# Kernel optimization log

Measured on AMD Instinct MI355X. Metric: run time of the kernel, lower is better.

The kernel has to match this reference:

```python
import jax, jax.numpy as jnp
import numpy as np

B, D, E, H1, H2 = 64, 2048, 64, 512, 256
EPS = 1e-5


def setup_inputs() -> dict:
    key = jax.random.key(0)
    ks = jax.random.split(key, 8)
    s = lambda k, shape, scale: jax.random.normal(k, shape, dtype=jnp.float32) * scale
    return {
        "sparse_representation": s(ks[0], (B, D), 1.0),
        "emb": s(ks[1], (D, E), 1.0),
        "W1": s(ks[2], (D + E, H1), (D + E) ** -0.5),
        "b1": s(ks[3], (H1,), 0.02),
        "g1": jnp.ones((H1,), jnp.float32),
        "beta1": jnp.zeros((H1,), jnp.float32),
        "m1": jnp.zeros((H1,), jnp.float32),
        "v1": jnp.ones((H1,), jnp.float32),
        "W2": s(ks[4], (H1, H2), H1 ** -0.5),
        "b2": s(ks[5], (H2,), 0.02),
        "g2": jnp.ones((H2,), jnp.float32),
        "beta2": jnp.zeros((H2,), jnp.float32),
        "m2": jnp.zeros((H2,), jnp.float32),
        "v2": jnp.ones((H2,), jnp.float32),
        "W3": s(ks[6], (H2, 1), H2 ** -0.5),
        "b3": s(ks[7], (1,), 0.02),
    }


def _bn_relu(x, g, beta, m, v):
    # eval-mode BatchNorm1d followed by ReLU
    return jax.nn.relu((x - m) * jax.lax.rsqrt(v + EPS) * g + beta)


def reference(sparse_representation, emb, W1, b1, g1, beta1, m1, v1,
              W2, b2, g2, beta2, m2, v2, W3, b3):
    rep = sparse_representation  # (B, D)
    W1d, W1e = W1[:D], W1[D:]    # (D, H1), (E, H1)
    # Fused predict_all: for each k, masked input zeros column k, so
    # Linear(masked_k) = rep @ W1d - rep[:, k] * W1d[k]
    base = rep @ W1d + b1                       # (B, H1)
    emb_h = emb @ W1e                           # (D, H1) per-index embedding contribution
    h1 = base[:, None, :] + emb_h[None, :, :] - rep[:, :, None] * W1d[None, :, :]  # (B, D, H1)
    h1 = _bn_relu(h1, g1, beta1, m1, v1)
    h2 = jnp.einsum("bkh,ho->bko", h1, W2) + b2  # (B, D, H2)
    h2 = _bn_relu(h2, g2, beta2, m2, v2)
    out = jnp.einsum("bkh,h->bk", h2, W3[:, 0]) + b3[0]  # (B, D)
    return out
```

## Files before the change

kernel.cpp:

```cpp
#include <hip/hip_runtime.h>

#define EPS 1e-5f

typedef __attribute__((ext_vector_type(8))) short short8;
typedef __attribute__((ext_vector_type(4))) float f32x4;

__device__ __forceinline__ float bflo(unsigned u) { return __uint_as_float(u << 16); }
__device__ __forceinline__ float bfhi(unsigned u) { return __uint_as_float(u & 0xffff0000u); }
__device__ __forceinline__ unsigned short f2bf(float f) {
  unsigned u = __float_as_uint(f);
  u = u + 0x7FFFu + ((u >> 16) & 1u);
  return (unsigned short)(u >> 16);
}
__device__ __forceinline__ unsigned pack2(float a, float b) {
  return (unsigned)f2bf(a) | ((unsigned)f2bf(b) << 16);
}

__global__ __launch_bounds__(256) void prep(
    const float* __restrict__ emb, const float* __restrict__ W1,
    const float* __restrict__ g1, const float* __restrict__ v1,
    const float* __restrict__ b1, const float* __restrict__ m1,
    const float* __restrict__ beta1,
    const float* __restrict__ W2,
    const float* __restrict__ g2, const float* __restrict__ v2,
    const float* __restrict__ b2, const float* __restrict__ m2,
    const float* __restrict__ beta2,
    unsigned* __restrict__ Q, unsigned* __restrict__ R,
    unsigned short* __restrict__ W2t,
    float* __restrict__ t2, float* __restrict__ c2, float* __restrict__ pbias) {
  const int x = blockIdx.x, t = threadIdx.x;
  if (x < 256) {
    const int k0 = x * 8;
    const int h = t * 2;
    const float a0 = g1[h] * rsqrtf(v1[h] + EPS);
    const float a1 = g1[h + 1] * rsqrtf(v1[h + 1] + EPS);
    const float* We = W1 + 2048 * 512;
    float acc0[8], acc1[8];
    #pragma unroll
    for (int k = 0; k < 8; ++k) { acc0[k] = 0.f; acc1[k] = 0.f; }
    for (int e = 0; e < 64; ++e) {
      float2 wv = *(const float2*)(We + e * 512 + h);
      #pragma unroll
      for (int k = 0; k < 8; ++k) {
        float ev = emb[(k0 + k) * 64 + e];
        acc0[k] = fmaf(ev, wv.x, acc0[k]);
        acc1[k] = fmaf(ev, wv.y, acc1[k]);
      }
    }
    #pragma unroll
    for (int k = 0; k < 8; ++k) {
      Q[(k0 + k) * 256 + t] = pack2(a0 * acc0[k], a1 * acc1[k]);
      float2 wv = *(const float2*)(W1 + (size_t)(k0 + k) * 512 + h);
      R[(k0 + k) * 256 + t] = pack2(a0 * wv.x, a1 * wv.y);
    }
  } else if (x < 320) {
    const int h0 = (x - 256) * 8;
    const int o = t;
    unsigned d[4];
    #pragma unroll
    for (int i = 0; i < 4; ++i) {
      float v0 = W2[(h0 + 2 * i) * 256 + o];
      float v1_ = W2[(h0 + 2 * i + 1) * 256 + o];
      d[i] = pack2(v0, v1_);
    }
    *(uint4*)(W2t + o * 512 + h0) = make_uint4(d[0], d[1], d[2], d[3]);
  } else {
    float tv = g2[t] * rsqrtf(v2[t] + EPS);
    t2[t] = tv;
    c2[t] = tv * (b2[t] - m2[t]) + beta2[t];
    #pragma unroll
    for (int i = 0; i < 2; ++i) {
      int h = t + i * 256;
      float a = g1[h] * rsqrtf(v1[h] + EPS);
      pbias[h] = a * (b1[h] - m1[h]) + beta1[h];
    }
  }
}

__global__ __launch_bounds__(1024) void p_gemm(
    const float* __restrict__ rep, const unsigned* __restrict__ R,
    const float* __restrict__ pbias, unsigned* __restrict__ P) {
  __shared__ float red[16 * 512];
  const int b = blockIdx.x, t = threadIdx.x;
  const int lane = t & 63, kq = t >> 6;
  const int hl = lane * 8;
  const float* rp = rep + b * 2048 + kq * 128;
  const unsigned* Rp = R + (size_t)(kq * 128) * 256 + lane * 4;
  float acc[8];
  #pragma unroll
  for (int i = 0; i < 8; ++i) acc[i] = 0.f;
  #pragma unroll 4
  for (int k = 0; k < 128; ++k) {
    uint4 rv = *(const uint4*)(Rp + (size_t)k * 256);
    float rk = rp[k];
    acc[0] = fmaf(rk, bflo(rv.x), acc[0]); acc[1] = fmaf(rk, bfhi(rv.x), acc[1]);
    acc[2] = fmaf(rk, bflo(rv.y), acc[2]); acc[3] = fmaf(rk, bfhi(rv.y), acc[3]);
    acc[4] = fmaf(rk, bflo(rv.z), acc[4]); acc[5] = fmaf(rk, bfhi(rv.z), acc[5]);
    acc[6] = fmaf(rk, bflo(rv.w), acc[6]); acc[7] = fmaf(rk, bfhi(rv.w), acc[7]);
  }
  *(f32x4*)(&red[kq * 512 + hl])     = (f32x4){acc[0], acc[1], acc[2], acc[3]};
  *(f32x4*)(&red[kq * 512 + hl + 4]) = (f32x4){acc[4], acc[5], acc[6], acc[7]};
  __syncthreads();
  if (t < 256) {
    const int h = t * 2;
    float s0 = 0.f, s1 = 0.f;
    #pragma unroll
    for (int q = 0; q < 16; ++q) { s0 += red[q * 512 + h]; s1 += red[q * 512 + h + 1]; }
    P[b * 256 + t] = pack2(s0 + pbias[h], s1 + pbias[h + 1]);
  }
}

__global__ __launch_bounds__(256, 2) void fused_main(
    const float* __restrict__ rep,
    const unsigned* __restrict__ P,
    const unsigned* __restrict__ Q,
    const unsigned* __restrict__ Rm,
    const unsigned short* __restrict__ W2t,
    const float* __restrict__ t2, const float* __restrict__ c2,
    const float* __restrict__ W3, const float* __restrict__ b3,
    float* __restrict__ out) {
  __shared__ unsigned short A_lds[2][8192];
  __shared__ float repc[128];
  __shared__ float partial[4][128];

  const int t = threadIdx.x;
  const int w = t >> 6;
  const int ln = t & 15;
  const int lq = (t >> 4) & 3;
  const int ks_id = w & 1;
  const int hi_id = w >> 1;
  const int k0 = blockIdx.x * 2;

  if (t < 128) repc[t] = rep[(t & 63) * 2048 + k0 + (t >> 6)];

  f32x4 acc[8][4];
  #pragma unroll
  for (int mi = 0; mi < 8; ++mi)
    #pragma unroll
    for (int nj = 0; nj < 4; ++nj) acc[mi][nj] = (f32x4){0.f, 0.f, 0.f, 0.f};

  __syncthreads();

  auto gen = [&](int c, unsigned short* buf) {
    const int colbase = c * 64 + ks_id * 32 + lq * 8;
    const int cb2 = colbase >> 1;
    #pragma unroll
    for (int p = 0; p < 4; ++p) {
      const int mi = p * 2 + hi_id;
      const int r = mi * 16 + ln;
      const int bb = r & 63;
      const int kg = k0 + (r >> 6);
      uint4 pv = *(const uint4*)(P + (bb << 8) + cb2);
      uint4 qv = *(const uint4*)(Q + (kg << 8) + cb2);
      uint4 rv = *(const uint4*)(Rm + (kg << 8) + cb2);
      const float rb = repc[r];
      unsigned d[4];
      {
        float z0 = fmaf(-rb, bflo(rv.x), bflo(pv.x) + bflo(qv.x));
        float z1 = fmaf(-rb, bfhi(rv.x), bfhi(pv.x) + bfhi(qv.x));
        d[0] = pack2(fmaxf(z0, 0.f), fmaxf(z1, 0.f));
        z0 = fmaf(-rb, bflo(rv.y), bflo(pv.y) + bflo(qv.y));
        z1 = fmaf(-rb, bfhi(rv.y), bfhi(pv.y) + bfhi(qv.y));
        d[1] = pack2(fmaxf(z0, 0.f), fmaxf(z1, 0.f));
        z0 = fmaf(-rb, bflo(rv.z), bflo(pv.z) + bflo(qv.z));
        z1 = fmaf(-rb, bfhi(rv.z), bfhi(pv.z) + bfhi(qv.z));
        d[2] = pack2(fmaxf(z0, 0.f), fmaxf(z1, 0.f));
        z0 = fmaf(-rb, bflo(rv.w), bflo(pv.w) + bflo(qv.w));
        z1 = fmaf(-rb, bfhi(rv.w), bfhi(pv.w) + bfhi(qv.w));
        d[3] = pack2(fmaxf(z0, 0.f), fmaxf(z1, 0.f));
      }
      *(uint4*)(&buf[(size_t)(p * 256 + t) * 8]) = make_uint4(d[0], d[1], d[2], d[3]);
    }
  };

  gen(0, A_lds[0]);

  for (int c = 0; c < 8; ++c) {
    __syncthreads();
    if (c < 7) gen(c + 1, A_lds[(c + 1) & 1]);
    const unsigned short* buf = A_lds[c & 1];
    #pragma unroll
    for (int ks = 0; ks < 2; ++ks) {
      short8 afr[8];
      #pragma unroll
      for (int mi = 0; mi < 8; ++mi)
        afr[mi] = *(const short8*)(buf + (size_t)((((mi * 2 + ks) * 4 + lq) * 16 + ln) * 8));
      short8 bfr[4];
      #pragma unroll
      for (int nj = 0; nj < 4; ++nj)
        bfr[nj] = *(const short8*)(W2t + (size_t)(w * 64 + nj * 16 + ln) * 512 + c * 64 + ks * 32 + lq * 8);
      #pragma unroll
      for (int mi = 0; mi < 8; ++mi)
        #pragma unroll
        for (int nj = 0; nj < 4; ++nj)
          acc[mi][nj] = __builtin_amdgcn_mfma_f32_16x16x32_bf16(afr[mi], bfr[nj], acc[mi][nj], 0, 0, 0);
    }
  }

  float t2v[4], c2v[4], w3v[4];
  #pragma unroll
  for (int nj = 0; nj < 4; ++nj) {
    int o = w * 64 + nj * 16 + ln;
    t2v[nj] = t2[o];
    c2v[nj] = c2[o];
    w3v[nj] = W3[o];
  }
  #pragma unroll
  for (int mi = 0; mi < 8; ++mi) {
    float s[4] = {0.f, 0.f, 0.f, 0.f};
    #pragma unroll
    for (int nj = 0; nj < 4; ++nj)
      #pragma unroll
      for (int r = 0; r < 4; ++r) {
        float u = fmaf(t2v[nj], acc[mi][nj][r], c2v[nj]);
        u = fmaxf(u, 0.f);
        s[r] = fmaf(u, w3v[nj], s[r]);
      }
    #pragma unroll
    for (int r = 0; r < 4; ++r) {
      #pragma unroll
      for (int m = 1; m < 16; m <<= 1) s[r] += __shfl_xor(s[r], m, 64);
    }
    if (ln == 0) {
      #pragma unroll
      for (int r = 0; r < 4; ++r) partial[w][mi * 16 + lq * 4 + r] = s[r];
    }
  }
  __syncthreads();
  if (t < 128) {
    out[(t & 63) * 2048 + k0 + (t >> 6)] =
        partial[0][t] + partial[1][t] + partial[2][t] + partial[3][t] + b3[0];
  }
}

extern "C" void kernel_launch(void* const* d_in, const int* in_sizes, int n_in,
                              void* d_out, int out_size, void* d_ws, size_t ws_size,
                              hipStream_t stream) {
  const float* rep   = (const float*)d_in[0];
  const float* emb   = (const float*)d_in[1];
  const float* W1    = (const float*)d_in[2];
  const float* b1    = (const float*)d_in[3];
  const float* g1    = (const float*)d_in[4];
  const float* beta1 = (const float*)d_in[5];
  const float* m1    = (const float*)d_in[6];
  const float* v1    = (const float*)d_in[7];
  const float* W2    = (const float*)d_in[8];
  const float* b2    = (const float*)d_in[9];
  const float* g2    = (const float*)d_in[10];
  const float* beta2 = (const float*)d_in[11];
  const float* m2    = (const float*)d_in[12];
  const float* v2    = (const float*)d_in[13];
  const float* W3    = (const float*)d_in[14];
  const float* b3    = (const float*)d_in[15];
  float* out = (float*)d_out;

  char* ws = (char*)d_ws;
  float* t2            = (float*)(ws + 0);
  float* c2            = (float*)(ws + 1024);
  float* pbias         = (float*)(ws + 2048);
  unsigned* P          = (unsigned*)(ws + 4096);
  unsigned* Q          = (unsigned*)(ws + 69632);
  unsigned* R          = (unsigned*)(ws + 2166784);
  unsigned short* W2t  = (unsigned short*)(ws + 4263936);

  prep<<<321, 256, 0, stream>>>(emb, W1, g1, v1, b1, m1, beta1, W2, g2, v2, b2, m2,
                                beta2, Q, R, W2t, t2, c2, pbias);
  p_gemm<<<64, 1024, 0, stream>>>(rep, R, pbias, P);
  fused_main<<<1024, 256, 0, stream>>>(rep, P, Q, R, W2t, t2, c2, W3, b3, out);
}
```

Baseline: 194.7 us.

## Merge P GEMM into prep kernel, fold bias into Q, widen main-loop K chunk

Removes the separate p_gemm launch by computing the rep@W1d product in fp32 inside the prep kernel, with 128 extra blocks each handling one batch row and one half of H1. The folded BN1 bias now goes into Q instead of P, and P stays fp32. The main kernel processes 128-column chunks (4 iterations instead of 8), with each wave owning one k-slice, which doubles the LDS staging buffer. This trades one launch and some per-chunk barriers for more LDS per block and a serial 2048-long dot product per thread in the new prep blocks.

Result: slower. 287.0 us (+47.4%).

```diff
diff --git a/kernel.cpp b/kernel.cpp
--- a/kernel.cpp
+++ b/kernel.cpp
@@ -16,8 +16,9 @@
   return (unsigned)f2bf(a) | ((unsigned)f2bf(b) << 16);
 }
 
-__global__ __launch_bounds__(256) void prep(
-    const float* __restrict__ emb, const float* __restrict__ W1,
+__global__ __launch_bounds__(256) void prep2(
+    const float* __restrict__ rep, const float* __restrict__ emb,
+    const float* __restrict__ W1,
     const float* __restrict__ g1, const float* __restrict__ v1,
     const float* __restrict__ b1, const float* __restrict__ m1,
     const float* __restrict__ beta1,
@@ -27,34 +28,40 @@
     const float* __restrict__ beta2,
     unsigned* __restrict__ Q, unsigned* __restrict__ R,
     unsigned short* __restrict__ W2t,
-    float* __restrict__ t2, float* __restrict__ c2, float* __restrict__ pbias) {
+    float* __restrict__ t2, float* __restrict__ c2, float* __restrict__ Pf) {
+  __shared__ float smem[2048];
   const int x = blockIdx.x, t = threadIdx.x;
-  if (x < 256) {
-    const int k0 = x * 8;
+  if (x < 512) {
+    const int k0 = x * 4;
+    smem[t] = emb[x * 256 + t];
+    __syncthreads();
     const int h = t * 2;
     const float a0 = g1[h] * rsqrtf(v1[h] + EPS);
     const float a1 = g1[h + 1] * rsqrtf(v1[h + 1] + EPS);
+    const float pb0 = a0 * (b1[h] - m1[h]) + beta1[h];
+    const float pb1 = a1 * (b1[h + 1] - m1[h + 1]) + beta1[h + 1];
     const float* We = W1 + 2048 * 512;
-    float acc0[8], acc1[8];
-    #pragma unroll
-    for (int k = 0; k < 8; ++k) { acc0[k] = 0.f; acc1[k] = 0.f; }
+    float acc0[4], acc1[4];
+    #pragma unroll
+    for (int k = 0; k < 4; ++k) { acc0[k] = 0.f; acc1[k] = 0.f; }
+    #pragma unroll 4
     for (int e = 0; e < 64; ++e) {
       float2 wv = *(const float2*)(We + e * 512 + h);
       #pragma unroll
-      for (int k = 0; k < 8; ++k) {
-        float ev = emb[(k0 + k) * 64 + e];
+      for (int k = 0; k < 4; ++k) {
+        float ev = smem[k * 64 + e];
         acc0[k] = fmaf(ev, wv.x, acc0[k]);
         acc1[k] = fmaf(ev, wv.y, acc1[k]);
       }
     }
     #pragma unroll
-    for (int k = 0; k < 8; ++k) {
-      Q[(k0 + k) * 256 + t] = pack2(a0 * acc0[k], a1 * acc1[k]);
+    for (int k = 0; k < 4; ++k) {
+      Q[(k0 + k) * 256 + t] = pack2(a0 * acc0[k] + pb0, a1 * acc1[k] + pb1);
       float2 wv = *(const float2*)(W1 + (size_t)(k0 + k) * 512 + h);
       R[(k0 + k) * 256 + t] = pack2(a0 * wv.x, a1 * wv.y);
     }
-  } else if (x < 320) {
-    const int h0 = (x - 256) * 8;
+  } else if (x < 576) {
+    const int h0 = (x - 512) * 8;
     const int o = t;
     unsigned d[4];
     #pragma unroll
@@ -64,62 +71,36 @@
       d[i] = pack2(v0, v1_);
     }
     *(uint4*)(W2t + o * 512 + h0) = make_uint4(d[0], d[1], d[2], d[3]);
+  } else if (x < 704) {
+    const int i = x - 576;
+    const int b = i >> 1, half = i & 1;
+    #pragma unroll
+    for (int j = 0; j < 8; ++j) smem[j * 256 + t] = rep[b * 2048 + j * 256 + t];
+    __syncthreads();
+    const int h = half * 256 + t;
+    const float ah = g1[h] * rsqrtf(v1[h] + EPS);
+    float acc = 0.f;
+    #pragma unroll 8
+    for (int k = 0; k < 2048; ++k)
+      acc = fmaf(smem[k], W1[(size_t)k * 512 + h], acc);
+    Pf[b * 512 + h] = ah * acc;
   } else {
     float tv = g2[t] * rsqrtf(v2[t] + EPS);
     t2[t] = tv;
     c2[t] = tv * (b2[t] - m2[t]) + beta2[t];
-    #pragma unroll
-    for (int i = 0; i < 2; ++i) {
-      int h = t + i * 256;
-      float a = g1[h] * rsqrtf(v1[h] + EPS);
-      pbias[h] = a * (b1[h] - m1[h]) + beta1[h];
-    }
-  }
-}
-
-__global__ __launch_bounds__(1024) void p_gemm(
-    const float* __restrict__ rep, const unsigned* __restrict__ R,
-    const float* __restrict__ pbias, unsigned* __restrict__ P) {
-  __shared__ float red[16 * 512];
-  const int b = blockIdx.x, t = threadIdx.x;
-  const int lane = t & 63, kq = t >> 6;
-  const int hl = lane * 8;
-  const float* rp = rep + b * 2048 + kq * 128;
-  const unsigned* Rp = R + (size_t)(kq * 128) * 256 + lane * 4;
-  float acc[8];
-  #pragma unroll
-  for (int i = 0; i < 8; ++i) acc[i] = 0.f;
-  #pragma unroll 4
-  for (int k = 0; k < 128; ++k) {
-    uint4 rv = *(const uint4*)(Rp + (size_t)k * 256);
-    float rk = rp[k];
-    acc[0] = fmaf(rk, bflo(rv.x), acc[0]); acc[1] = fmaf(rk, bfhi(rv.x), acc[1]);
-    acc[2] = fmaf(rk, bflo(rv.y), acc[2]); acc[3] = fmaf(rk, bfhi(rv.y), acc[3]);
-    acc[4] = fmaf(rk, bflo(rv.z), acc[4]); acc[5] = fmaf(rk, bfhi(rv.z), acc[5]);
-    acc[6] = fmaf(rk, bflo(rv.w), acc[6]); acc[7] = fmaf(rk, bfhi(rv.w), acc[7]);
-  }
-  *(f32x4*)(&red[kq * 512 + hl])     = (f32x4){acc[0], acc[1], acc[2], acc[3]};
-  *(f32x4*)(&red[kq * 512 + hl + 4]) = (f32x4){acc[4], acc[5], acc[6], acc[7]};
-  __syncthreads();
-  if (t < 256) {
-    const int h = t * 2;
-    float s0 = 0.f, s1 = 0.f;
-    #pragma unroll
-    for (int q = 0; q < 16; ++q) { s0 += red[q * 512 + h]; s1 += red[q * 512 + h + 1]; }
-    P[b * 256 + t] = pack2(s0 + pbias[h], s1 + pbias[h + 1]);
   }
 }
 
 __global__ __launch_bounds__(256, 2) void fused_main(
     const float* __restrict__ rep,
-    const unsigned* __restrict__ P,
+    const float* __restrict__ Pf,
     const unsigned* __restrict__ Q,
     const unsigned* __restrict__ Rm,
     const unsigned short* __restrict__ W2t,
     const float* __restrict__ t2, const float* __restrict__ c2,
     const float* __restrict__ W3, const float* __restrict__ b3,
     float* __restrict__ out) {
-  __shared__ unsigned short A_lds[2][8192];
+  __shared__ unsigned short A_lds[2][16384];
   __shared__ float repc[128];
   __shared__ float partial[4][128];
 
@@ -127,8 +108,7 @@
   const int w = t >> 6;
   const int ln = t & 15;
   const int lq = (t >> 4) & 3;
-  const int ks_id = w & 1;
-  const int hi_id = w >> 1;
+  const int ks_g = w;
   const int k0 = blockIdx.x * 2;
 
   if (t < 128) repc[t] = rep[(t & 63) * 2048 + k0 + (t >> 6)];
@@ -142,53 +122,55 @@
   __syncthreads();
 
   auto gen = [&](int c, unsigned short* buf) {
-    const int colbase = c * 64 + ks_id * 32 + lq * 8;
-    const int cb2 = colbase >> 1;
-    #pragma unroll
-    for (int p = 0; p < 4; ++p) {
-      const int mi = p * 2 + hi_id;
+    const int col = c * 128 + ks_g * 32 + lq * 8;
+    const int cb2 = col >> 1;
+    #pragma unroll
+    for (int p = 0; p < 8; ++p) {
+      const int mi = p;
       const int r = mi * 16 + ln;
       const int bb = r & 63;
       const int kg = k0 + (r >> 6);
-      uint4 pv = *(const uint4*)(P + (bb << 8) + cb2);
-      uint4 qv = *(const uint4*)(Q + (kg << 8) + cb2);
-      uint4 rv = *(const uint4*)(Rm + (kg << 8) + cb2);
+      const float4 pv0 = *(const float4*)(Pf + bb * 512 + col);
+      const float4 pv1 = *(const float4*)(Pf + bb * 512 + col + 4);
+      const uint4 qv = *(const uint4*)(Q + (kg << 8) + cb2);
+      const uint4 rv = *(const uint4*)(Rm + (kg << 8) + cb2);
       const float rb = repc[r];
       unsigned d[4];
       {
-        float z0 = fmaf(-rb, bflo(rv.x), bflo(pv.x) + bflo(qv.x));
-        float z1 = fmaf(-rb, bfhi(rv.x), bfhi(pv.x) + bfhi(qv.x));
+        float z0 = fmaf(-rb, bflo(rv.x), pv0.x + bflo(qv.x));
+        float z1 = fmaf(-rb, bfhi(rv.x), pv0.y + bfhi(qv.x));
         d[0] = pack2(fmaxf(z0, 0.f), fmaxf(z1, 0.f));
-        z0 = fmaf(-rb, bflo(rv.y), bflo(pv.y) + bflo(qv.y));
-        z1 = fmaf(-rb, bfhi(rv.y), bfhi(pv.y) + bfhi(qv.y));
+        z0 = fmaf(-rb, bflo(rv.y), pv0.z + bflo(qv.y));
+        z1 = fmaf(-rb, bfhi(rv.y), pv0.w + bfhi(qv.y));
         d[1] = pack2(fmaxf(z0, 0.f), fmaxf(z1, 0.f));
-        z0 = fmaf(-rb, bflo(rv.z), bflo(pv.z) + bflo(qv.z));
-        z1 = fmaf(-rb, bfhi(rv.z), bfhi(pv.z) + bfhi(qv.z));
+        z0 = fmaf(-rb, bflo(rv.z), pv1.x + bflo(qv.z));
+        z1 = fmaf(-rb, bfhi(rv.z), pv1.y + bfhi(qv.z));
         d[2] = pack2(fmaxf(z0, 0.f), fmaxf(z1, 0.f));
-        z0 = fmaf(-rb, bflo(rv.w), bflo(pv.w) + bflo(qv.w));
-        z1 = fmaf(-rb, bfhi(rv.w), bfhi(pv.w) + bfhi(qv.w));
+        z0 = fmaf(-rb, bflo(rv.w), pv1.z + bflo(qv.w));
+        z1 = fmaf(-rb, bfhi(rv.w), pv1.w + bfhi(qv.w));
         d[3] = pack2(fmaxf(z0, 0.f), fmaxf(z1, 0.f));
       }
-      *(uint4*)(&buf[(size_t)(p * 256 + t) * 8]) = make_uint4(d[0], d[1], d[2], d[3]);
+      *(uint4*)(&buf[(size_t)((((mi * 4 + ks_g) * 4 + lq) * 16 + ln)) * 8]) =
+          make_uint4(d[0], d[1], d[2], d[3]);
     }
   };
 
   gen(0, A_lds[0]);
 
-  for (int c = 0; c < 8; ++c) {
+  for (int c = 0; c < 4; ++c) {
     __syncthreads();
-    if (c < 7) gen(c + 1, A_lds[(c + 1) & 1]);
+    if (c < 3) gen(c + 1, A_lds[(c + 1) & 1]);
     const unsigned short* buf = A_lds[c & 1];
     #pragma unroll
-    for (int ks = 0; ks < 2; ++ks) {
+    for (int ks = 0; ks < 4; ++ks) {
       short8 afr[8];
       #pragma unroll
       for (int mi = 0; mi < 8; ++mi)
-        afr[mi] = *(const short8*)(buf + (size_t)((((mi * 2 + ks) * 4 + lq) * 16 + ln) * 8));
+        afr[mi] = *(const short8*)(buf + (size_t)((((mi * 4 + ks) * 4 + lq) * 16 + ln) * 8));
       short8 bfr[4];
       #pragma unroll
       for (int nj = 0; nj < 4; ++nj)
-        bfr[nj] = *(const short8*)(W2t + (size_t)(w * 64 + nj * 16 + ln) * 512 + c * 64 + ks * 32 + lq * 8);
+        bfr[nj] = *(const short8*)(W2t + (size_t)(w * 64 + nj * 16 + ln) * 512 + c * 128 + ks * 32 + lq * 8);
       #pragma unroll
       for (int mi = 0; mi < 8; ++mi)
         #pragma unroll
@@ -255,16 +237,14 @@
   float* out = (float*)d_out;
 
   char* ws = (char*)d_ws;
-  float* t2            = (float*)(ws + 0);
-  float* c2            = (float*)(ws + 1024);
-  float* pbias         = (float*)(ws + 2048);
-  unsigned* P          = (unsigned*)(ws + 4096);
-  unsigned* Q          = (unsigned*)(ws + 69632);
-  unsigned* R          = (unsigned*)(ws + 2166784);
-  unsigned short* W2t  = (unsigned short*)(ws + 4263936);
-
-  prep<<<321, 256, 0, stream>>>(emb, W1, g1, v1, b1, m1, beta1, W2, g2, v2, b2, m2,
-                                beta2, Q, R, W2t, t2, c2, pbias);
-  p_gemm<<<64, 1024, 0, stream>>>(rep, R, pbias, P);
-  fused_main<<<1024, 256, 0, stream>>>(rep, P, Q, R, W2t, t2, c2, W3, b3, out);
-}
+  float* Pf            = (float*)(ws + 0);
+  unsigned* Q          = (unsigned*)(ws + 131072);
+  unsigned* R          = (unsigned*)(ws + 2228224);
+  unsigned short* W2t  = (unsigned short*)(ws + 4325376);
+  float* t2            = (float*)(ws + 4587520);
+  float* c2            = (float*)(ws + 4588544);
+
+  prep2<<<705, 256, 0, stream>>>(rep, emb, W1, g1, v1, b1, m1, beta1, W2, g2, v2,
+                                 b2, m2, beta2, Q, R, W2t, t2, c2, Pf);
+  fused_main<<<1024, 256, 0, stream>>>(rep, Pf, Q, R, W2t, t2, c2, W3, b3, out);
+}
```

## Split A generation into separate kernel materialized in workspace, atomic split-K p_gemm

Applied to the files above, without the earlier changes.

When the workspace is large enough, this adds a path that writes the full bf16 hidden-1 activation tensor (128 MB) to global memory in a dedicated genA kernel. A separate gemmA kernel then streams it into LDS with global_load_lds and runs the MFMA GEMM without elementwise generation work in its inner loop. p_gemm is split across 512 blocks that accumulate with float atomics into a zeroed fp32 P buffer, and prep is widened. The trade is a large extra global write and read of the activation tensor in exchange for decoupling generation from the MFMA loop and adding parallelism. If the workspace is too small, the old three-kernel path runs.

Result: slower. 226.7 us (+16.4%).

```diff
diff --git a/kernel.cpp b/kernel.cpp
--- a/kernel.cpp
+++ b/kernel.cpp
@@ -15,8 +15,249 @@
 __device__ __forceinline__ unsigned pack2(float a, float b) {
   return (unsigned)f2bf(a) | ((unsigned)f2bf(b) << 16);
 }
-
-__global__ __launch_bounds__(256) void prep(
+__device__ __forceinline__ void g2lds16(const void* g, void* l) {
+  __builtin_amdgcn_global_load_lds(
+      (const __attribute__((address_space(1))) unsigned*)g,
+      (__attribute__((address_space(3))) unsigned*)l, 16, 0, 0);
+}
+
+
+__global__ __launch_bounds__(256) void prep2(
+    const float* __restrict__ emb, const float* __restrict__ W1,
+    const float* __restrict__ g1, const float* __restrict__ v1,
+    const float* __restrict__ b1, const float* __restrict__ m1,
+    const float* __restrict__ beta1,
+    const float* __restrict__ W2,
+    const float* __restrict__ g2, const float* __restrict__ v2,
+    const float* __restrict__ b2, const float* __restrict__ m2,
+    const float* __restrict__ beta2,
+    unsigned* __restrict__ Q, unsigned* __restrict__ R,
+    unsigned short* __restrict__ W2t,
+    float* __restrict__ t2, float* __restrict__ c2, float* __restrict__ Pf) {
+  __shared__ float smem[256];
+  const int x = blockIdx.x, t = threadIdx.x;
+  if (x < 512) {
+    const int k0 = x * 4;
+    smem[t] = emb[x * 256 + t];
+    __syncthreads();
+    const int h = t * 2;
+    const float a0 = g1[h] * rsqrtf(v1[h] + EPS);
+    const float a1 = g1[h + 1] * rsqrtf(v1[h + 1] + EPS);
+    const float pb0 = a0 * (b1[h] - m1[h]) + beta1[h];
+    const float pb1 = a1 * (b1[h + 1] - m1[h + 1]) + beta1[h + 1];
+    const float* We = W1 + 2048 * 512;
+    float acc0[4], acc1[4];
+    #pragma unroll
+    for (int k = 0; k < 4; ++k) { acc0[k] = 0.f; acc1[k] = 0.f; }
+    #pragma unroll 4
+    for (int e = 0; e < 64; ++e) {
+      float2 wv = *(const float2*)(We + e * 512 + h);
+      #pragma unroll
+      for (int k = 0; k < 4; ++k) {
+        float ev = smem[k * 64 + e];
+        acc0[k] = fmaf(ev, wv.x, acc0[k]);
+        acc1[k] = fmaf(ev, wv.y, acc1[k]);
+      }
+    }
+    #pragma unroll
+    for (int k = 0; k < 4; ++k) {
+      Q[(k0 + k) * 256 + t] = pack2(a0 * acc0[k] + pb0, a1 * acc1[k] + pb1);
+      float2 wv = *(const float2*)(W1 + (size_t)(k0 + k) * 512 + h);
+      R[(k0 + k) * 256 + t] = pack2(a0 * wv.x, a1 * wv.y);
+    }
+  } else if (x < 576) {
+    const int h0 = (x - 512) * 8;
+    const int o = t;
+    unsigned d[4];
+    #pragma unroll
+    for (int i = 0; i < 4; ++i) {
+      float v0 = W2[(h0 + 2 * i) * 256 + o];
+      float v1_ = W2[(h0 + 2 * i + 1) * 256 + o];
+      d[i] = pack2(v0, v1_);
+    }
+    *(uint4*)(W2t + o * 512 + h0) = make_uint4(d[0], d[1], d[2], d[3]);
+  } else {
+    float tv = g2[t] * rsqrtf(v2[t] + EPS);
+    t2[t] = tv;
+    c2[t] = tv * (b2[t] - m2[t]) + beta2[t];
+    f32x4 z = (f32x4){0.f, 0.f, 0.f, 0.f};
+    #pragma unroll 8
+    for (int j = 0; j < 32; ++j)
+      *(f32x4*)(Pf + ((size_t)(j * 256 + t)) * 4) = z;
+  }
+}
+
+__global__ __launch_bounds__(256) void p_gemm(
+    const float* __restrict__ rep, const unsigned* __restrict__ R,
+    float* __restrict__ Pf) {
+  __shared__ float red[4][512];
+  const int b = blockIdx.x >> 3, ksl = blockIdx.x & 7;
+  const int t = threadIdx.x, lane = t & 63, kq = t >> 6;
+  const int kbase = ksl * 256 + kq * 64;
+  const unsigned* Rp = R + (size_t)kbase * 256 + lane * 4;
+  const float* rp = rep + b * 2048 + kbase;
+  float acc[8];
+  #pragma unroll
+  for (int i = 0; i < 8; ++i) acc[i] = 0.f;
+  #pragma unroll 8
+  for (int k = 0; k < 64; ++k) {
+    uint4 rv = *(const uint4*)(Rp + (size_t)k * 256);
+    float rk = rp[k];
+    acc[0] = fmaf(rk, bflo(rv.x), acc[0]); acc[1] = fmaf(rk, bfhi(rv.x), acc[1]);
+    acc[2] = fmaf(rk, bflo(rv.y), acc[2]); acc[3] = fmaf(rk, bfhi(rv.y), acc[3]);
+    acc[4] = fmaf(rk, bflo(rv.z), acc[4]); acc[5] = fmaf(rk, bfhi(rv.z), acc[5]);
+    acc[6] = fmaf(rk, bflo(rv.w), acc[6]); acc[7] = fmaf(rk, bfhi(rv.w), acc[7]);
+  }
+  *(f32x4*)(&red[kq][lane * 8])     = (f32x4){acc[0], acc[1], acc[2], acc[3]};
+  *(f32x4*)(&red[kq][lane * 8 + 4]) = (f32x4){acc[4], acc[5], acc[6], acc[7]};
+  __syncthreads();
+  {
+    const int h = t * 2;
+    float s0 = red[0][h] + red[1][h] + red[2][h] + red[3][h];
+    float s1 = red[0][h + 1] + red[1][h + 1] + red[2][h + 1] + red[3][h + 1];
+    atomicAdd(&Pf[b * 512 + h], s0);
+    atomicAdd(&Pf[b * 512 + h + 1], s1);
+  }
+}
+
+__global__ __launch_bounds__(256) void genA(
+    const float* __restrict__ rep, const float* __restrict__ Pf,
+    const unsigned* __restrict__ Q, const unsigned* __restrict__ Rm,
+    unsigned* __restrict__ A) {
+  const int t = threadIdx.x;
+  const int kp = blockIdx.x;
+  const int w = t >> 6, ln = t & 15, lq = (t >> 4) & 3;
+  const int ks_id = w & 1, hi_id = w >> 1;
+  const int k0 = kp * 2;
+  float rb[4];
+  #pragma unroll
+  for (int p = 0; p < 4; ++p) {
+    int r = (p * 2 + hi_id) * 16 + ln;
+    rb[p] = rep[(r & 63) * 2048 + k0 + (r >> 6)];
+  }
+  unsigned* Ab = A + (size_t)kp * 32768;
+  #pragma unroll 1
+  for (int c = 0; c < 8; ++c) {
+    const int col = c * 64 + ks_id * 32 + lq * 8;
+    const int cb2 = col >> 1;
+    #pragma unroll
+    for (int p = 0; p < 4; ++p) {
+      const int r = (p * 2 + hi_id) * 16 + ln;
+      const int bb = r & 63;
+      const int kg = k0 + (r >> 6);
+      const float4 pv0 = *(const float4*)(Pf + bb * 512 + col);
+      const float4 pv1 = *(const float4*)(Pf + bb * 512 + col + 4);
+      const uint4 qv = *(const uint4*)(Q + (kg << 8) + cb2);
+      const uint4 rv = *(const uint4*)(Rm + (kg << 8) + cb2);
+      const float rp_ = rb[p];
+      unsigned d[4];
+      float z0, z1;
+      z0 = fmaf(-rp_, bflo(rv.x), pv0.x + bflo(qv.x));
+      z1 = fmaf(-rp_, bfhi(rv.x), pv0.y + bfhi(qv.x));
+      d[0] = pack2(fmaxf(z0, 0.f), fmaxf(z1, 0.f));
+      z0 = fmaf(-rp_, bflo(rv.y), pv0.z + bflo(qv.y));
+      z1 = fmaf(-rp_, bfhi(rv.y), pv0.w + bfhi(qv.y));
+      d[1] = pack2(fmaxf(z0, 0.f), fmaxf(z1, 0.f));
+      z0 = fmaf(-rp_, bflo(rv.z), pv1.x + bflo(qv.z));
+      z1 = fmaf(-rp_, bfhi(rv.z), pv1.y + bfhi(qv.z));
+      d[2] = pack2(fmaxf(z0, 0.f), fmaxf(z1, 0.f));
+      z0 = fmaf(-rp_, bflo(rv.w), pv1.z + bflo(qv.w));
+      z1 = fmaf(-rp_, bfhi(rv.w), pv1.w + bfhi(qv.w));
+      d[3] = pack2(fmaxf(z0, 0.f), fmaxf(z1, 0.f));
+      *(uint4*)(Ab + (size_t)(c * 1024 + p * 256 + t) * 4) =
+          make_uint4(d[0], d[1], d[2], d[3]);
+    }
+  }
+}
+
+__global__ __launch_bounds__(256, 2) void gemmA(
+    const unsigned* __restrict__ A,
+    const unsigned short* __restrict__ W2t,
+    const float* __restrict__ t2, const float* __restrict__ c2,
+    const float* __restrict__ W3, const float* __restrict__ b3,
+    float* __restrict__ out) {
+  __shared__ unsigned short A_lds[2][8192];
+  __shared__ float partial[4][128];
+  const int t = threadIdx.x;
+  const int w = t >> 6, ln = t & 15, lq = (t >> 4) & 3;
+  const int l = t & 63;
+  const int kp = blockIdx.x, k0 = kp * 2;
+  const unsigned* Ab = A + (size_t)kp * 32768;
+
+  f32x4 acc[8][4];
+  #pragma unroll
+  for (int mi = 0; mi < 8; ++mi)
+    #pragma unroll
+    for (int nj = 0; nj < 4; ++nj) acc[mi][nj] = (f32x4){0.f, 0.f, 0.f, 0.f};
+
+  auto stage = [&](int c, int bi) {
+    const unsigned* src = Ab + (size_t)c * 4096 + (w * 64 + l) * 4;
+    #pragma unroll
+    for (int i = 0; i < 4; ++i)
+      g2lds16(src + i * 1024, &A_lds[bi][(size_t)(i * 256 + w * 64) * 8]);
+  };
+
+  stage(0, 0);
+
+  for (int c = 0; c < 8; ++c) {
+    __syncthreads();
+    if (c < 7) stage(c + 1, (c + 1) & 1);
+    const unsigned short* buf = A_lds[c & 1];
+    #pragma unroll
+    for (int ks = 0; ks < 2; ++ks) {
+      short8 afr[8];
+      #pragma unroll
+      for (int mi = 0; mi < 8; ++mi)
+        afr[mi] = *(const short8*)(buf + (size_t)((((mi * 2 + ks) * 4 + lq) * 16 + ln) * 8));
+      short8 bfr[4];
+      #pragma unroll
+      for (int nj = 0; nj < 4; ++nj)
+        bfr[nj] = *(const short8*)(W2t + (size_t)(w * 64 + nj * 16 + ln) * 512 + c * 64 + ks * 32 + lq * 8);
+      #pragma unroll
+      for (int mi = 0; mi < 8; ++mi)
+        #pragma unroll
+        for (int nj = 0; nj < 4; ++nj)
+          acc[mi][nj] = __builtin_amdgcn_mfma_f32_16x16x32_bf16(afr[mi], bfr[nj], acc[mi][nj], 0, 0, 0);
+    }
+  }
+
+  float t2v[4], c2v[4], w3v[4];
+  #pragma unroll
+  for (int nj = 0; nj < 4; ++nj) {
+    int o = w * 64 + nj * 16 + ln;
+    t2v[nj] = t2[o];
+    c2v[nj] = c2[o];
+    w3v[nj] = W3[o];
+  }
+  #pragma unroll
+  for (int mi = 0; mi < 8; ++mi) {
+    float s[4] = {0.f, 0.f, 0.f, 0.f};
+    #pragma unroll
+    for (int nj = 0; nj < 4; ++nj)
+      #pragma unroll
+      for (int r = 0; r < 4; ++r) {
+        float u = fmaf(t2v[nj], acc[mi][nj][r], c2v[nj]);
+        u = fmaxf(u, 0.f);
+        s[r] = fmaf(u, w3v[nj], s[r]);
+      }
+    #pragma unroll
+    for (int r = 0; r < 4; ++r) {
+      #pragma unroll
+      for (int m = 1; m < 16; m <<= 1) s[r] += __shfl_xor(s[r], m, 64);
+    }
+    if (ln == 0) {
+      #pragma unroll
+      for (int r = 0; r < 4; ++r) partial[w][mi * 16 + lq * 4 + r] = s[r];
+    }
+  }
+  __syncthreads();
+  if (t < 128) {
+    out[(t & 63) * 2048 + k0 + (t >> 6)] =
+        partial[0][t] + partial[1][t] + partial[2][t] + partial[3][t] + b3[0];
+  }
+}
+
+__global__ __launch_bounds__(256) void prep_v1(
     const float* __restrict__ emb, const float* __restrict__ W1,
     const float* __restrict__ g1, const float* __restrict__ v1,
     const float* __restrict__ b1, const float* __restrict__ m1,
@@ -77,7 +318,7 @@
   }
 }
 
-__global__ __launch_bounds__(1024) void p_gemm(
+__global__ __launch_bounds__(1024) void p_gemm_v1(
     const float* __restrict__ rep, const unsigned* __restrict__ R,
     const float* __restrict__ pbias, unsigned* __restrict__ P) {
   __shared__ float red[16 * 512];
@@ -110,7 +351,7 @@
   }
 }
 
-__global__ __launch_bounds__(256, 2) void fused_main(
+__global__ __launch_bounds__(256, 2) void fused_main_v1(
     const float* __restrict__ rep,
     const unsigned* __restrict__ P,
     const unsigned* __restrict__ Q,
@@ -122,7 +363,6 @@
   __shared__ unsigned short A_lds[2][8192];
   __shared__ float repc[128];
   __shared__ float partial[4][128];
-
   const int t = threadIdx.x;
   const int w = t >> 6;
   const int ln = t & 15;
@@ -130,17 +370,13 @@
   const int ks_id = w & 1;
   const int hi_id = w >> 1;
   const int k0 = blockIdx.x * 2;
-
   if (t < 128) repc[t] = rep[(t & 63) * 2048 + k0 + (t >> 6)];
-
   f32x4 acc[8][4];
   #pragma unroll
   for (int mi = 0; mi < 8; ++mi)
     #pragma unroll
     for (int nj = 0; nj < 4; ++nj) acc[mi][nj] = (f32x4){0.f, 0.f, 0.f, 0.f};
-
   __syncthreads();
-
   auto gen = [&](int c, unsigned short* buf) {
     const int colbase = c * 64 + ks_id * 32 + lq * 8;
     const int cb2 = colbase >> 1;
@@ -172,9 +408,7 @@
       *(uint4*)(&buf[(size_t)(p * 256 + t) * 8]) = make_uint4(d[0], d[1], d[2], d[3]);
     }
   };
-
   gen(0, A_lds[0]);
-
   for (int c = 0; c < 8; ++c) {
     __syncthreads();
     if (c < 7) gen(c + 1, A_lds[(c + 1) & 1]);
@@ -196,7 +430,6 @@
           acc[mi][nj] = __builtin_amdgcn_mfma_f32_16x16x32_bf16(afr[mi], bfr[nj], acc[mi][nj], 0, 0, 0);
     }
   }
-
   float t2v[4], c2v[4], w3v[4];
   #pragma unroll
   for (int nj = 0; nj < 4; ++nj) {
@@ -253,18 +486,37 @@
   const float* W3    = (const float*)d_in[14];
   const float* b3    = (const float*)d_in[15];
   float* out = (float*)d_out;
-
   char* ws = (char*)d_ws;
-  float* t2            = (float*)(ws + 0);
-  float* c2            = (float*)(ws + 1024);
-  float* pbias         = (float*)(ws + 2048);
-  unsigned* P          = (unsigned*)(ws + 4096);
-  unsigned* Q          = (unsigned*)(ws + 69632);
-  unsigned* R          = (unsigned*)(ws + 2166784);
-  unsigned short* W2t  = (unsigned short*)(ws + 4263936);
-
-  prep<<<321, 256, 0, stream>>>(emb, W1, g1, v1, b1, m1, beta1, W2, g2, v2, b2, m2,
-                                beta2, Q, R, W2t, t2, c2, pbias);
-  p_gemm<<<64, 1024, 0, stream>>>(rep, R, pbias, P);
-  fused_main<<<1024, 256, 0, stream>>>(rep, P, Q, R, W2t, t2, c2, W3, b3, out);
-}
+
+  const size_t A_OFF = 4589568;
+  const size_t NEED = A_OFF + (size_t)134217728;
+
+  if (ws_size >= NEED) {
+    float* Pf            = (float*)(ws + 0);
+    unsigned* Q          = (unsigned*)(ws + 131072);
+    unsigned* R          = (unsigned*)(ws + 2228224);
+    unsigned short* W2t  = (unsigned short*)(ws + 4325376);
+    float* t2            = (float*)(ws + 4587520);
+    float* c2            = (float*)(ws + 4588544);
+    unsigned* A          = (unsigned*)(ws + A_OFF);
+
+    prep2<<<577, 256, 0, stream>>>(emb, W1, g1, v1, b1, m1, beta1, W2, g2, v2,
+                                   b2, m2, beta2, Q, R, W2t, t2, c2, Pf);
+    p_gemm<<<512, 256, 0, stream>>>(rep, R, Pf);
+    genA<<<1024, 256, 0, stream>>>(rep, Pf, Q, R, A);
+    gemmA<<<1024, 256, 0, stream>>>(A, W2t, t2, c2, W3, b3, out);
+  } else {
+    float* t2            = (float*)(ws + 0);
+    float* c2            = (float*)(ws + 1024);
+    float* pbias         = (float*)(ws + 2048);
+    unsigned* P          = (unsigned*)(ws + 4096);
+    unsigned* Q          = (unsigned*)(ws + 69632);
+    unsigned* R          = (unsigned*)(ws + 2166784);
+    unsigned short* W2t  = (unsigned short*)(ws + 4263936);
+
+    prep_v1<<<321, 256, 0, stream>>>(emb, W1, g1, v1, b1, m1, beta1, W2, g2, v2,
+                                     b2, m2, beta2, Q, R, W2t, t2, c2, pbias);
+    p_gemm_v1<<<64, 1024, 0, stream>>>(rep, R, pbias, P);
+    fused_main_v1<<<1024, 256, 0, stream>>>(rep, P, Q, R, W2t, t2, c2, W3, b3, out);
+  }
+}
```
